# Kernel tuning notes

Measured on AMD Instinct MI355X. Metric: run time of the kernel, lower is better.

## Reference

```python
import jax, jax.numpy as jnp
import numpy as np

N, IN_DIM, OUT_DIM, HEADS = 8192, 256, 64, 2

def setup_inputs() -> dict:
    key = jax.random.key(0)
    k1, k2, k3, k4, k5 = jax.random.split(key, 5)
    x = jax.random.normal(k1, (N, IN_DIM), dtype=jnp.float32)
    adj = jax.random.randint(k2, (N, N), 0, 2, dtype=jnp.int32)
    # nn.Linear(in_dim, out_dim*heads, bias=False): weight [out_dim*heads, in_dim]
    W = jax.random.normal(k3, (OUT_DIM * HEADS, IN_DIM), dtype=jnp.float32) / np.sqrt(IN_DIM)
    attn_l = jax.random.normal(k4, (HEADS, OUT_DIM), dtype=jnp.float32)
    attn_r = jax.random.normal(k5, (HEADS, OUT_DIM), dtype=jnp.float32)
    return {"x": x, "adj": adj, "W": W, "attn_l": attn_l, "attn_r": attn_r}

def reference(x, adj, W, attn_l, attn_r):
    n = x.shape[0]
    h = (x @ W.T).reshape(n, HEADS, OUT_DIM)          # [N, H, D]
    el = jnp.einsum('nhd,hd->nh', h, attn_l)           # [N, H]
    er = jnp.einsum('nhd,hd->nh', h, attn_r)           # [N, H]
    e = el[:, None, :] + er[None, :, :]                # [N, N, H]
    e = jnp.where(adj[:, :, None] == 0, -jnp.inf, e)
    a = jax.nn.softmax(e, axis=1)                      # softmax over source nodes j
    out = jnp.einsum('ijh,jhd->ihd', a, h)             # [N, H, D]
    return out.reshape(n, HEADS * OUT_DIM)
```

## Files before the change

kernel.cpp:

```cpp
#include <hip/hip_runtime.h>
#include <cstdint>
#include <cstddef>

#define N_NODES 8192
#define IN_DIM  256
#define OUT_DIM 64
#define HEADS   2
#define FEAT    128
#define NTILES  9
#define ACC_STRIDE 132
#define KSPLIT  8

typedef __bf16 bf16x8 __attribute__((ext_vector_type(8)));
typedef float  f32x4  __attribute__((ext_vector_type(4)));
typedef int    i32x4  __attribute__((ext_vector_type(4)));
typedef unsigned uu32x4 __attribute__((ext_vector_type(4)));

static __device__ __forceinline__ unsigned short f2bf(float f) {
  unsigned u = __float_as_uint(f);
  u += 0x7FFFu + ((u >> 16) & 1u);
  return (unsigned short)(u >> 16);
}

__global__ __launch_bounds__(256) void k_pack(const int* __restrict__ adj,
                                              unsigned long long* __restrict__ bm64) {
  const int tid = threadIdx.x;
  const int wv = tid >> 6, lane = tid & 63;
  const int row = blockIdx.x * 4 + wv;
  const i32x4* rp = (const i32x4*)(adj + (size_t)row * N_NODES) + lane;
  unsigned long long* op = bm64 + (size_t)row * 128;

  for (int c = 0; c < 32; c += 8) {
    i32x4 v[8];
#pragma unroll
    for (int i = 0; i < 8; ++i)
      v[i] = __builtin_nontemporal_load(rp + (size_t)(c + i) * 64);
#pragma unroll
    for (int i = 0; i < 8; ++i) {
      unsigned long long m0 = __ballot(v[i][0] != 0);
      unsigned long long m1 = __ballot(v[i][1] != 0);
      unsigned long long m2 = __ballot(v[i][2] != 0);
      unsigned long long m3 = __ballot(v[i][3] != 0);
      unsigned long long mv = (lane == 0) ? m0 : (lane == 1) ? m1
                            : (lane == 2) ? m2 : m3;
      if (lane < 4) op[(c + i) * 4 + lane] = mv;
    }
  }
}

__global__ __launch_bounds__(256) void k_prep(const float* __restrict__ x,
                                              const float* __restrict__ W,
                                              const float* __restrict__ attn_r,
                                              uint4* __restrict__ frag) {
  const int kb = blockIdx.x;
  const int tid = threadIdx.x;
  const int tx = tid & 15, ty = tid >> 4;
  const int j0 = kb * 32;

  __shared__ float xs[32][68];
  __shared__ float wl[128][68];
  __shared__ unsigned short pk[32][146];

  float acc[2][8] = {};

  for (int kc = 0; kc < IN_DIM; kc += 64) {
    __syncthreads();
#pragma unroll
    for (int p = 0; p < 2; p++) {
      const int slot = p*256 + tid;
      const int r = slot >> 4, k4 = slot & 15;
      *(float4*)&xs[r][k4*4] = *(const float4*)(x + (size_t)(j0 + r)*IN_DIM + kc + k4*4);
    }
#pragma unroll
    for (int p = 0; p < 8; p++) {
      const int slot = p*256 + tid;
      const int r = slot >> 4, k4 = slot & 15;
      *(float4*)&wl[r][k4*4] = *(const float4*)(W + (size_t)r*IN_DIM + kc + k4*4);
    }
    __syncthreads();
#pragma unroll
    for (int k4 = 0; k4 < 16; k4++) {
      float4 xr[2], wr[8];
#pragma unroll
      for (int i = 0; i < 2; i++) xr[i] = *(const float4*)&xs[ty + i*16][k4*4];
#pragma unroll
      for (int jj = 0; jj < 8; jj++) wr[jj] = *(const float4*)&wl[tx + jj*16][k4*4];
#pragma unroll
      for (int i = 0; i < 2; i++)
#pragma unroll
        for (int jj = 0; jj < 8; jj++)
          acc[i][jj] += xr[i].x*wr[jj].x + xr[i].y*wr[jj].y +
                        xr[i].z*wr[jj].z + xr[i].w*wr[jj].w;
    }
  }

  float ar[8];
#pragma unroll
  for (int jj = 0; jj < 8; jj++)
    ar[jj] = attn_r[((jj >> 2)) * OUT_DIM + ((tx + jj*16) & 63)];
  float e0[2] = {}, e1[2] = {};
#pragma unroll
  for (int i = 0; i < 2; i++) {
#pragma unroll
    for (int jj = 0; jj < 4; jj++) e0[i] += acc[i][jj] * ar[jj];
#pragma unroll
    for (int jj = 4; jj < 8; jj++) e1[i] += acc[i][jj] * ar[jj];
  }
#pragma unroll
  for (int m = 1; m <= 8; m <<= 1) {
#pragma unroll
    for (int i = 0; i < 2; i++) {
      e0[i] += __shfl_xor(e0[i], m);
      e1[i] += __shfl_xor(e1[i], m);
    }
  }
  float w0[2], w1[2];
#pragma unroll
  for (int i = 0; i < 2; i++) { w0[i] = __expf(e0[i]); w1[i] = __expf(e1[i]); }

#pragma unroll
  for (int i = 0; i < 2; i++) {
    const int row = ty + i*16;
#pragma unroll
    for (int jj = 0; jj < 8; jj++)
      pk[row][tx + jj*16] = f2bf((jj < 4 ? w0[i] : w1[i]) * acc[i][jj]);
    pk[row][128 + tx] = (tx == 0) ? f2bf(w0[i]) : (tx == 1) ? f2bf(w1[i]) : 0;
  }
  __syncthreads();

#pragma unroll
  for (int t = 0; t < 3; t++) {
    const int wid = t*256 + tid;
    if (wid < 576) {
      const int l = wid & 63, n = wid >> 6;
      const int col = n*16 + (l & 15), jb = (l >> 4) * 8;
      uint4 o;
      o.x = (unsigned)pk[jb+0][col] | ((unsigned)pk[jb+1][col] << 16);
      o.y = (unsigned)pk[jb+2][col] | ((unsigned)pk[jb+3][col] << 16);
      o.z = (unsigned)pk[jb+4][col] | ((unsigned)pk[jb+5][col] << 16);
      o.w = (unsigned)pk[jb+6][col] | ((unsigned)pk[jb+7][col] << 16);
      frag[((size_t)kb*NTILES + n)*64 + l] = o;
    }
  }
}

__global__ __launch_bounds__(256, 2) void k_main(const unsigned long long* __restrict__ bm64,
                                                 const uint4* __restrict__ fragB,
                                                 float* __restrict__ accum) {
  const int mb = blockIdx.x >> 3;
  const int ks = blockIdx.x & 7;
  const int tid = threadIdx.x;
  const int wave = tid >> 6, lane = tid & 63;
  const int m16 = lane & 15, quad = lane >> 4;
  const int q2 = quad * 2;

  const int row0 = mb*128 + wave*32 + m16;
  const i32x4* a0p = (const i32x4*)((const char*)bm64 + (size_t)row0*1024 + ks*128);
  const i32x4* a1p = a0p + 1024;
  const uu32x4* bb = (const uu32x4*)fragB + (size_t)(ks*32)*NTILES*64 + lane;

  f32x4 acc0[NTILES], acc1[NTILES];
#pragma unroll
  for (int n = 0; n < NTILES; n++) {
    acc0[n] = (f32x4){0.f, 0.f, 0.f, 0.f};
    acc1[n] = (f32x4){0.f, 0.f, 0.f, 0.f};
  }

  uu32x4 bvA[NTILES], bvB[NTILES];

  auto unpack = [&](unsigned w0, unsigned w1, unsigned w2, unsigned w3,
                    int s) -> bf16x8 {
    const unsigned t0 = (w0 >> s) & 3u;
    const unsigned t1 = (w1 >> s) & 3u;
    const unsigned t2 = (w2 >> s) & 3u;
    const unsigned t3 = (w3 >> s) & 3u;
    unsigned u0 = (t0 & 1u ? 0x3F80u : 0u) | (t1 & 1u ? 0x3F800000u : 0u);
    unsigned u1 = (t2 & 1u ? 0x3F80u : 0u) | (t3 & 1u ? 0x3F800000u : 0u);
    unsigned u2 = (t0 & 2u ? 0x3F80u : 0u) | (t1 & 2u ? 0x3F800000u : 0u);
    unsigned u3 = (t2 & 2u ? 0x3F80u : 0u) | (t3 & 2u ? 0x3F800000u : 0u);
    uu32x4 u = {u0, u1, u2, u3};
    return __builtin_bit_cast(bf16x8, u);
  };

  i32x4 c0a = a0p[0], c0b = a0p[1];
  i32x4 c1a = a1p[0], c1b = a1p[1];
#pragma unroll
  for (int t = 0; t < NTILES; t++) bvA[t] = bb[(size_t)t*64];

  for (int g = 0; g < 4; ++g) {
    i32x4 n0a = a0p[(g + 1)*2],     n0b = a0p[(g + 1)*2 + 1];
    i32x4 n1a = a1p[(g + 1)*2],     n1b = a1p[(g + 1)*2 + 1];
#pragma unroll
    for (int j = 0; j < 8; ++j) {
      const int kk = g*8 + j;
      const uu32x4* bp = bb + (size_t)(kk + 1)*NTILES*64;
      if ((j & 1) == 0) {
#pragma unroll
        for (int t = 0; t < NTILES; t++) bvB[t] = bp[(size_t)t*64];
      } else {
#pragma unroll
        for (int t = 0; t < NTILES; t++) bvA[t] = bp[(size_t)t*64];
      }
      const int s = (j & 3)*8 + q2;
      bf16x8 af0, af1;
      if (j < 4) {
        af0 = unpack((unsigned)c0a[0], (unsigned)c0a[2],
                     (unsigned)c0b[0], (unsigned)c0b[2], s);
        af1 = unpack((unsigned)c1a[0], (unsigned)c1a[2],
                     (unsigned)c1b[0], (unsigned)c1b[2], s);
      } else {
        af0 = unpack((unsigned)c0a[1], (unsigned)c0a[3],
                     (unsigned)c0b[1], (unsigned)c0b[3], s);
        af1 = unpack((unsigned)c1a[1], (unsigned)c1a[3],
                     (unsigned)c1b[1], (unsigned)c1b[3], s);
      }
      const uu32x4* bv = ((j & 1) == 0) ? bvA : bvB;
#pragma unroll
      for (int n = 0; n < NTILES; n++) {
        bf16x8 bfr = __builtin_bit_cast(bf16x8, bv[n]);
        acc0[n] = __builtin_amdgcn_mfma_f32_16x16x32_bf16(af0, bfr, acc0[n], 0, 0, 0);
      }
#pragma unroll
      for (int n = 0; n < NTILES; n++) {
        bf16x8 bfr = __builtin_bit_cast(bf16x8, bv[n]);
        acc1[n] = __builtin_amdgcn_mfma_f32_16x16x32_bf16(af1, bfr, acc1[n], 0, 0, 0);
      }
    }
    c0a = n0a; c0b = n0b; c1a = n1a; c1b = n1b;
  }

  const int rb0 = mb*128 + wave*32 + quad*4;
  float* op = accum + (size_t)ks*N_NODES*ACC_STRIDE;
#pragma unroll
  for (int n = 0; n < NTILES; n++) {
    if (n == 8 && m16 >= HEADS) continue;
#pragma unroll
    for (int r = 0; r < 4; r++) {
      op[(size_t)(rb0 + r)*ACC_STRIDE + n*16 + m16]      = acc0[n][r];
      op[(size_t)(rb0 + 16 + r)*ACC_STRIDE + n*16 + m16] = acc1[n][r];
    }
  }
}

__global__ void k_div(const float* __restrict__ acc, float* __restrict__ out) {
  const int tid = threadIdx.x;
  const int r = tid >> 5, c4 = (tid & 31) << 2;
  const int i = blockIdx.x * 8 + r;
  const int h = c4 >> 6;
  f32x4 num = (f32x4){0.f, 0.f, 0.f, 0.f};
  float den = 0.f;
#pragma unroll
  for (int s = 0; s < KSPLIT; s++) {
    const float* p = acc + ((size_t)s*N_NODES + i)*ACC_STRIDE;
    num += *(const f32x4*)(p + c4);
    den += p[FEAT + h];
  }
  f32x4 o = num / (f32x4){den, den, den, den};
  *(f32x4*)(out + (size_t)i*FEAT + c4) = o;
}

extern "C" void kernel_launch(void* const* d_in, const int* in_sizes, int n_in,
                              void* d_out, int out_size, void* d_ws, size_t ws_size,
                              hipStream_t stream) {
  const float* x      = (const float*)d_in[0];
  const int*   adj    = (const int*)  d_in[1];
  const float* W      = (const float*)d_in[2];
  const float* attn_r = (const float*)d_in[4];

  char* ws = (char*)d_ws;
  uint4*              frag = (uint4*)(ws + 0);
  unsigned long long* bm64 = (unsigned long long*)(ws + (4u << 20));
  float*              acc  = (float*)(ws + (16u << 20));
  float*              out  = (float*)d_out;

  hipLaunchKernelGGL(k_pack, dim3(2048), dim3(256), 0, stream, adj, bm64);
  hipLaunchKernelGGL(k_prep, dim3(256),  dim3(256), 0, stream, x, W, attn_r, frag);
  hipLaunchKernelGGL(k_main, dim3(512),  dim3(256), 0, stream, bm64, frag, acc);
  hipLaunchKernelGGL(k_div,  dim3(1024), dim3(256), 0, stream, acc, out);
}
```

Measured before the change: 413.4 us.

## Give each wave 64 rows in main kernel to double B-fragment reuse

```diff
diff --git a/kernel.cpp b/kernel.cpp
--- a/kernel.cpp
+++ b/kernel.cpp
@@ -144,7 +144,7 @@
   }
 }
 
-__global__ __launch_bounds__(256, 2) void k_main(const unsigned long long* __restrict__ bm64,
+__global__ __launch_bounds__(128, 1) void k_main(const unsigned long long* __restrict__ bm64,
                                                  const uint4* __restrict__ fragB,
                                                  float* __restrict__ accum) {
   const int mb = blockIdx.x >> 3;
@@ -154,19 +154,19 @@
   const int m16 = lane & 15, quad = lane >> 4;
   const int q2 = quad * 2;
 
-  const int row0 = mb*128 + wave*32 + m16;
-  const i32x4* a0p = (const i32x4*)((const char*)bm64 + (size_t)row0*1024 + ks*128);
-  const i32x4* a1p = a0p + 1024;
+  const int row0 = mb*128 + wave*64 + m16;
+  const char* abase = (const char*)bm64 + (size_t)row0*1024 + ks*128;
   const uu32x4* bb = (const uu32x4*)fragB + (size_t)(ks*32)*NTILES*64 + lane;
 
-  f32x4 acc0[NTILES], acc1[NTILES];
-#pragma unroll
-  for (int n = 0; n < NTILES; n++) {
-    acc0[n] = (f32x4){0.f, 0.f, 0.f, 0.f};
-    acc1[n] = (f32x4){0.f, 0.f, 0.f, 0.f};
-  }
+  f32x4 acc[4][NTILES];
+#pragma unroll
+  for (int s = 0; s < 4; s++)
+#pragma unroll
+    for (int n = 0; n < NTILES; n++) acc[s][n] = (f32x4){0.f, 0.f, 0.f, 0.f};
 
   uu32x4 bvA[NTILES], bvB[NTILES];
+  i32x4 cA[4], cB[4];
+  i32x4 nA[4], nB[4];
 
   auto unpack = [&](unsigned w0, unsigned w1, unsigned w2, unsigned w3,
                     int s) -> bf16x8 {
@@ -182,14 +182,21 @@
     return __builtin_bit_cast(bf16x8, u);
   };
 
-  i32x4 c0a = a0p[0], c0b = a0p[1];
-  i32x4 c1a = a1p[0], c1b = a1p[1];
+#pragma unroll
+  for (int s = 0; s < 4; s++) {
+    const i32x4* p = (const i32x4*)(abase + s*16384);
+    cA[s] = p[0]; cB[s] = p[1];
+  }
 #pragma unroll
   for (int t = 0; t < NTILES; t++) bvA[t] = bb[(size_t)t*64];
 
   for (int g = 0; g < 4; ++g) {
-    i32x4 n0a = a0p[(g + 1)*2],     n0b = a0p[(g + 1)*2 + 1];
-    i32x4 n1a = a1p[(g + 1)*2],     n1b = a1p[(g + 1)*2 + 1];
+    __builtin_amdgcn_s_barrier();
+#pragma unroll
+    for (int s = 0; s < 4; s++) {
+      const i32x4* p = (const i32x4*)(abase + s*16384 + (g + 1)*32);
+      nA[s] = p[0]; nB[s] = p[1];
+    }
 #pragma unroll
     for (int j = 0; j < 8; ++j) {
       const int kk = g*8 + j;
@@ -201,43 +208,40 @@
 #pragma unroll
         for (int t = 0; t < NTILES; t++) bvA[t] = bp[(size_t)t*64];
       }
-      const int s = (j & 3)*8 + q2;
-      bf16x8 af0, af1;
-      if (j < 4) {
-        af0 = unpack((unsigned)c0a[0], (unsigned)c0a[2],
-                     (unsigned)c0b[0], (unsigned)c0b[2], s);
-        af1 = unpack((unsigned)c1a[0], (unsigned)c1a[2],
-                     (unsigned)c1b[0], (unsigned)c1b[2], s);
-      } else {
-        af0 = unpack((unsigned)c0a[1], (unsigned)c0a[3],
-                     (unsigned)c0b[1], (unsigned)c0b[3], s);
-        af1 = unpack((unsigned)c1a[1], (unsigned)c1a[3],
-                     (unsigned)c1b[1], (unsigned)c1b[3], s);
+      const int sh = (j & 3)*8 + q2;
+      bf16x8 af[4];
+#pragma unroll
+      for (int s = 0; s < 4; s++) {
+        if (j < 4)
+          af[s] = unpack((unsigned)cA[s][0], (unsigned)cA[s][2],
+                         (unsigned)cB[s][0], (unsigned)cB[s][2], sh);
+        else
+          af[s] = unpack((unsigned)cA[s][1], (unsigned)cA[s][3],
+                         (unsigned)cB[s][1], (unsigned)cB[s][3], sh);
       }
       const uu32x4* bv = ((j & 1) == 0) ? bvA : bvB;
 #pragma unroll
-      for (int n = 0; n < NTILES; n++) {
-        bf16x8 bfr = __builtin_bit_cast(bf16x8, bv[n]);
-        acc0[n] = __builtin_amdgcn_mfma_f32_16x16x32_bf16(af0, bfr, acc0[n], 0, 0, 0);
-      }
-#pragma unroll
-      for (int n = 0; n < NTILES; n++) {
-        bf16x8 bfr = __builtin_bit_cast(bf16x8, bv[n]);
-        acc1[n] = __builtin_amdgcn_mfma_f32_16x16x32_bf16(af1, bfr, acc1[n], 0, 0, 0);
-      }
-    }
-    c0a = n0a; c0b = n0b; c1a = n1a; c1b = n1b;
-  }
-
-  const int rb0 = mb*128 + wave*32 + quad*4;
+      for (int s = 0; s < 4; s++)
+#pragma unroll
+        for (int n = 0; n < NTILES; n++) {
+          bf16x8 bfr = __builtin_bit_cast(bf16x8, bv[n]);
+          acc[s][n] = __builtin_amdgcn_mfma_f32_16x16x32_bf16(af[s], bfr, acc[s][n], 0, 0, 0);
+        }
+    }
+#pragma unroll
+    for (int s = 0; s < 4; s++) { cA[s] = nA[s]; cB[s] = nB[s]; }
+  }
+
   float* op = accum + (size_t)ks*N_NODES*ACC_STRIDE;
 #pragma unroll
-  for (int n = 0; n < NTILES; n++) {
-    if (n == 8 && m16 >= HEADS) continue;
-#pragma unroll
-    for (int r = 0; r < 4; r++) {
-      op[(size_t)(rb0 + r)*ACC_STRIDE + n*16 + m16]      = acc0[n][r];
-      op[(size_t)(rb0 + 16 + r)*ACC_STRIDE + n*16 + m16] = acc1[n][r];
+  for (int s = 0; s < 4; s++) {
+    const int rb = mb*128 + wave*64 + s*16 + quad*4;
+#pragma unroll
+    for (int n = 0; n < NTILES; n++) {
+      if (n == 8 && m16 >= HEADS) continue;
+#pragma unroll
+      for (int r = 0; r < 4; r++)
+        op[(size_t)(rb + r)*ACC_STRIDE + n*16 + m16] = acc[s][n][r];
     }
   }
 }
@@ -275,6 +279,6 @@
 
   hipLaunchKernelGGL(k_pack, dim3(2048), dim3(256), 0, stream, adj, bm64);
   hipLaunchKernelGGL(k_prep, dim3(256),  dim3(256), 0, stream, x, W, attn_r, frag);
-  hipLaunchKernelGGL(k_main, dim3(512),  dim3(256), 0, stream, bm64, frag, acc);
+  hipLaunchKernelGGL(k_main, dim3(512),  dim3(128), 0, stream, bm64, frag, acc);
   hipLaunchKernelGGL(k_div,  dim3(1024), dim3(256), 0, stream, acc, out);
 }
```

Result: no change. 408.8 us (median of 2 runs) (-1.1%).
